# Kernel optimization log

Hardware: AMD Instinct MI355X
Metric: run time of the kernel (lower is better)

Reference implementation:

```python
import jax, jax.numpy as jnp
import numpy as np

N = 100000   # nodes
E = 640000   # edges
D = 128      # feature dim
G = 512      # graphs in the batch


def setup_inputs() -> dict:
    key = jax.random.key(0)
    ks = jax.random.split(key, 6)
    x = jax.random.normal(ks[0], (N, D), dtype=jnp.float32)
    edge_index = jax.random.randint(ks[1], (2, E), 0, N, dtype=jnp.int32)
    batch = jnp.sort(jax.random.randint(ks[2], (N,), 0, G, dtype=jnp.int32))
    scale = 1.0 / np.sqrt(D)
    W0 = jax.random.normal(ks[3], (D, D), dtype=jnp.float32) * scale
    W1 = jax.random.normal(ks[4], (D, D), dtype=jnp.float32) * scale
    W2 = jax.random.normal(ks[5], (D, D), dtype=jnp.float32) * scale
    return {"x": x, "edge_index": edge_index, "batch": batch,
            "W0": W0, "W1": W1, "W2": W2}


def gcn_conv(x, W, row, col, n):
    """GCNConv (bias=False): x' = D^-1/2 (A + I) D^-1/2 (x @ W).
    row/col already include self-loops."""
    xw = x @ W                                              # [N, D]
    deg = jax.ops.segment_sum(jnp.ones_like(col, dtype=x.dtype), col,
                              num_segments=n)               # [N]
    dinv = jnp.where(deg > 0, jax.lax.rsqrt(deg), 0.0)
    norm = dinv[row] * dinv[col]                            # [E+N]
    msgs = norm[:, None] * xw[row]                          # gather + scale
    return jax.ops.segment_sum(msgs, col, num_segments=n)   # scatter-add


def reference(x, edge_index, batch, W0, W1, W2):
    n = x.shape[0]
    loops = jnp.arange(n, dtype=edge_index.dtype)
    row = jnp.concatenate([edge_index[0], loops])
    col = jnp.concatenate([edge_index[1], loops])
    # conv_layers[:-1] (no activation between them in forward)
    x = gcn_conv(x, W0, row, col, n)
    x = gcn_conv(x, W1, row, col, n)
    x = jax.nn.leaky_relu(x, negative_slope=0.01)
    x = gcn_conv(x, W2, row, col, n)
    # global_add_pool over graph ids
    return jax.ops.segment_sum(x, batch, num_segments=G)    # [G, D]
```

## Files before the change

kernel.cpp:

```cpp
#include <hip/hip_runtime.h>
#include <hip/hip_bf16.h>
#include <type_traits>

#define FEAT 128

typedef unsigned int uint32;
typedef unsigned short ushort16;
typedef __attribute__((ext_vector_type(8))) short short8;
typedef __attribute__((ext_vector_type(4))) float v4f;
typedef __attribute__((ext_vector_type(2))) float f32x2;

__device__ __forceinline__ ushort16 f2bf(float f) {
    uint32 u = __float_as_uint(f);
    u += 0x7fffu + ((u >> 16) & 1u);
    return (ushort16)(u >> 16);
}
__device__ __forceinline__ float bflo(uint32 u) { return __uint_as_float(u << 16); }
__device__ __forceinline__ float bfhi(uint32 u) { return __uint_as_float(u & 0xffff0000u); }
__device__ __forceinline__ f32x2 up2(uint32 u) { return (f32x2){bflo(u), bfhi(u)}; }

__global__ __launch_bounds__(256) void hydra_kernel(const int* __restrict__ col,
                                                    int* __restrict__ counts,
                                                    const float* __restrict__ W0,
                                                    const float* __restrict__ W1,
                                                    ushort16* __restrict__ W01t,
                                                    float* __restrict__ Pbuf,
                                                    int histBlocks, int E) {
    int b = blockIdx.x;
    int t = threadIdx.x;
    if (b < histBlocks) {
        int id = b * 256 + t;
        if (id * 4 + 3 < E) {
            int4 c4 = *(const int4*)(col + id * 4);
            atomicAdd(&counts[c4.x], 1);
            atomicAdd(&counts[c4.y], 1);
            atomicAdd(&counts[c4.z], 1);
            atomicAdd(&counts[c4.w], 1);
        } else {
            for (int e = id * 4; e < E; e++) atomicAdd(&counts[col[e]], 1);
        }
    } else if (b < histBlocks + 64) {
        __shared__ float sW0[2][FEAT];
        int wb = b - histBlocks;
        int lk = t >> 7;
        int ncol = t & 127;
        int k = wb * 2 + lk;
        sW0[lk][ncol] = W0[(size_t)k * FEAT + ncol];
        __syncthreads();
        float acc = 0.f;
#pragma unroll 4
        for (int j = 0; j < FEAT; j++)
            acc += sW0[lk][j] * W1[(size_t)j * FEAT + ncol];
        W01t[(size_t)ncol * FEAT + k] = f2bf(acc);
    } else {
        int zb = b - histBlocks - 64;
        float4 z = make_float4(0.f, 0.f, 0.f, 0.f);
        float* p = Pbuf + (size_t)zb * 2048 + t * 8;
        *(float4*)p = z;
        *(float4*)(p + 4) = z;
    }
}

__global__ __launch_bounds__(256) void scan_part(const int* __restrict__ counts,
                                                 int* __restrict__ bsum, int n) {
    __shared__ int s[256];
    int base = blockIdx.x * 1024;
    int t = threadIdx.x;
    int v = 0;
#pragma unroll
    for (int i = 0; i < 4; i++) {
        int idx = base + t * 4 + i;
        if (idx < n) v += counts[idx];
    }
    s[t] = v;
    __syncthreads();
    for (int o = 128; o > 0; o >>= 1) {
        if (t < o) s[t] += s[t + o];
        __syncthreads();
    }
    if (t == 0) bsum[blockIdx.x] = s[0];
}

__global__ __launch_bounds__(256) void scan_final(const int* __restrict__ counts,
                                                  const int* __restrict__ bsum,
                                                  int* __restrict__ off, int* __restrict__ nxt,
                                                  float* __restrict__ dinv, int n, int nb) {
    __shared__ int s[256];
    __shared__ int sb[128];
    int base = blockIdx.x * 1024;
    int t = threadIdx.x;
    if (t < nb) sb[t] = bsum[t];
    int c[4];
    int sum = 0;
#pragma unroll
    for (int i = 0; i < 4; i++) {
        int idx = base + t * 4 + i;
        c[i] = (idx < n) ? counts[idx] : 0;
        sum += c[i];
    }
    int v0 = sum;
    s[t] = sum;
    __syncthreads();
    for (int o = 1; o < 256; o <<= 1) {
        int v = (t >= o) ? s[t - o] : 0;
        __syncthreads();
        s[t] += v;
        __syncthreads();
    }
    int blockBase = 0;
    for (int j = 0; j < blockIdx.x; j++) blockBase += sb[j];
    int excl = s[t] - v0 + blockBase;
#pragma unroll
    for (int i = 0; i < 4; i++) {
        int idx = base + t * 4 + i;
        if (idx < n) {
            off[idx] = excl;
            nxt[idx] = excl;
            dinv[idx] = rsqrtf((float)(c[i] + 1));
        }
        excl += c[i];
    }
    if (blockIdx.x == gridDim.x - 1 && t == 255) off[n] = excl;
}

__global__ void fill_kernel(const int* __restrict__ row, const int* __restrict__ col,
                            int* __restrict__ nxt,
                            int* __restrict__ srcArr, int E) {
    int e = blockIdx.x * 256 + threadIdx.x;
    if (e < E) {
        int c = col[e], r = row[e];
        int p = atomicAdd(&nxt[c], 1);
        __builtin_nontemporal_store(r, &srcArr[p]);
    }
}

template <typename T>
__global__ __launch_bounds__(256) void gemm_mfma(const T* __restrict__ A,
                                                 const ushort16* __restrict__ Wt,
                                                 ushort16* __restrict__ Ch, int n,
                                                 int leaky) {
    const int t = threadIdx.x;
    const int w = t >> 6;
    const int lane = t & 63;
    const int quad = lane >> 4;
    const int l16 = lane & 15;
    const int colBase = (w & 1) * 64;

    short8 wf[4][4];
#pragma unroll
    for (int ct = 0; ct < 4; ct++) {
        const ushort16* wp = Wt + (size_t)(colBase + ct * 16 + l16) * FEAT + quad * 8;
#pragma unroll
        for (int ks = 0; ks < 4; ks++) wf[ct][ks] = *(const short8*)(wp + ks * 32);
    }

    const int nTiles = (n + 15) >> 4;
    const int tStride = gridDim.x * 2;
    int tile = blockIdx.x * 2 + (w >> 1);
    if (tile >= nTiles) return;

    auto loadA = [&](int tl, short8 (&a)[4]) {
        const int row = tl * 16 + l16;
        if (row < n) {
            if constexpr (std::is_same<T, float>::value) {
#pragma unroll
                for (int ks = 0; ks < 4; ks++) {
                    const float* ap = A + (size_t)row * FEAT + quad * 8 + ks * 32;
                    float4 f0 = *(const float4*)ap;
                    float4 f1 = *(const float4*)(ap + 4);
                    short8 v;
                    v[0] = f2bf(f0.x); v[1] = f2bf(f0.y); v[2] = f2bf(f0.z); v[3] = f2bf(f0.w);
                    v[4] = f2bf(f1.x); v[5] = f2bf(f1.y); v[6] = f2bf(f1.z); v[7] = f2bf(f1.w);
                    a[ks] = v;
                }
            } else {
                const ushort16* ap = A + (size_t)row * FEAT + quad * 8;
#pragma unroll
                for (int ks = 0; ks < 4; ks++) a[ks] = *(const short8*)(ap + ks * 32);
            }
        } else {
#pragma unroll
            for (int ks = 0; ks < 4; ks++) a[ks] = (short8)0;
        }
    };

    short8 aCur[4];
    loadA(tile, aCur);

    while (tile < nTiles) {
        const int nextTile = tile + tStride;
        short8 aNxt[4];
        if (nextTile < nTiles) loadA(nextTile, aNxt);

        v4f acc[4];
#pragma unroll
        for (int ct = 0; ct < 4; ct++) acc[ct] = (v4f)0.f;
#pragma unroll
        for (int ct = 0; ct < 4; ct++)
#pragma unroll
            for (int ks = 0; ks < 4; ks++)
                acc[ct] = __builtin_amdgcn_mfma_f32_16x16x32_bf16(wf[ct][ks], aCur[ks], acc[ct], 0, 0, 0);

        const int row = tile * 16 + l16;
        if (row < n) {
#pragma unroll
            for (int ct = 0; ct < 4; ct++) {
                float p0 = acc[ct][0], p1 = acc[ct][1], p2 = acc[ct][2], p3 = acc[ct][3];
                if (leaky) {
                    p0 = (p0 >= 0.f) ? p0 : 0.01f * p0;
                    p1 = (p1 >= 0.f) ? p1 : 0.01f * p1;
                    p2 = (p2 >= 0.f) ? p2 : 0.01f * p2;
                    p3 = (p3 >= 0.f) ? p3 : 0.01f * p3;
                }
                uint2 o;
                o.x = (uint32)f2bf(p0) | ((uint32)f2bf(p1) << 16);
                o.y = (uint32)f2bf(p2) | ((uint32)f2bf(p3) << 16);
                *(uint2*)(Ch + (size_t)row * FEAT + colBase + ct * 16 + quad * 4) = o;
            }
        }

        tile = nextTile;
#pragma unroll
        for (int ks = 0; ks < 4; ks++) aCur[ks] = aNxt[ks];
    }
}

__global__ __launch_bounds__(256) void gather_kernel(const int* __restrict__ off,
                                                     const int* __restrict__ srcArr,
                                                     const float* __restrict__ dinv,
                                                     const ushort16* __restrict__ XWh,
                                                     ushort16* __restrict__ Hh, int n,
                                                     int leaky) {
    int node = blockIdx.x * 4 + (threadIdx.x >> 6);
    if (node >= n) return;
    int lane = threadIdx.x & 63;
    int grp = lane >> 4;
    int l16 = lane & 15;
    float dc = dinv[node];
    const uint4* table = (const uint4*)XWh;

    f32x2 acc[4];
    if (grp == 0) {
        uint4 v = table[(size_t)node * 16 + l16];
        f32x2 w0 = (f32x2){dc * dc, dc * dc};
        acc[0] = w0 * up2(v.x);
        acc[1] = w0 * up2(v.y);
        acc[2] = w0 * up2(v.z);
        acc[3] = w0 * up2(v.w);
    } else {
#pragma unroll
        for (int j = 0; j < 4; j++) acc[j] = (f32x2){0.f, 0.f};
    }

    int s = off[node], e = off[node + 1];
    int i = s + grp;
    for (; i + 4 < e; i += 8) {
        int r0 = srcArr[i];
        int r1 = srcArr[i + 4];
        uint4 u0 = table[(size_t)r0 * 16 + l16];
        uint4 u1 = table[(size_t)r1 * 16 + l16];
        float f0 = dc * dinv[r0];
        float f1 = dc * dinv[r1];
        f32x2 n0 = (f32x2){f0, f0};
        f32x2 n1 = (f32x2){f1, f1};
        acc[0] += n0 * up2(u0.x);
        acc[1] += n0 * up2(u0.y);
        acc[2] += n0 * up2(u0.z);
        acc[3] += n0 * up2(u0.w);
        acc[0] += n1 * up2(u1.x);
        acc[1] += n1 * up2(u1.y);
        acc[2] += n1 * up2(u1.z);
        acc[3] += n1 * up2(u1.w);
    }
    if (i < e) {
        int r0 = srcArr[i];
        uint4 u0 = table[(size_t)r0 * 16 + l16];
        float f0 = dc * dinv[r0];
        f32x2 n0 = (f32x2){f0, f0};
        acc[0] += n0 * up2(u0.x);
        acc[1] += n0 * up2(u0.y);
        acc[2] += n0 * up2(u0.z);
        acc[3] += n0 * up2(u0.w);
    }

    float b[8] = {acc[0].x, acc[0].y, acc[1].x, acc[1].y,
                  acc[2].x, acc[2].y, acc[3].x, acc[3].y};
#pragma unroll
    for (int j = 0; j < 8; j++) {
        b[j] += __shfl_xor(b[j], 16);
        b[j] += __shfl_xor(b[j], 32);
    }

    if (grp == 0) {
        if (leaky) {
#pragma unroll
            for (int j = 0; j < 8; j++) b[j] = (b[j] >= 0.f) ? b[j] : 0.01f * b[j];
        }
        uint4 o;
        o.x = (uint32)f2bf(b[0]) | ((uint32)f2bf(b[1]) << 16);
        o.y = (uint32)f2bf(b[2]) | ((uint32)f2bf(b[3]) << 16);
        o.z = (uint32)f2bf(b[4]) | ((uint32)f2bf(b[5]) << 16);
        o.w = (uint32)f2bf(b[6]) | ((uint32)f2bf(b[7]) << 16);
        *(uint4*)(Hh + (size_t)node * FEAT + l16 * 8) = o;
    }
}

__global__ __launch_bounds__(128) void pool_kernel(const ushort16* __restrict__ H,
                                                   const int* __restrict__ batch,
                                                   float* __restrict__ P, int n) {
    int t = threadIdx.x;
    int i0 = blockIdx.x * 64;
    if (i0 >= n) return;
    int i1 = min(i0 + 64, n);
    float acc = 0.f;
    int g = batch[i0];
    for (int i = i0; i < i1; i++) {
        int b = batch[i];
        if (b != g) {
            atomicAdd(&P[(size_t)g * FEAT + t], acc);
            acc = 0.f;
            g = b;
        }
        uint32 u = (uint32)(unsigned short)H[(size_t)i * FEAT + t];
        acc += __uint_as_float(u << 16);
    }
    atomicAdd(&P[(size_t)g * FEAT + t], acc);
}

__global__ __launch_bounds__(128) void pgemm_kernel(const float* __restrict__ P,
                                                    const float* __restrict__ W2,
                                                    float* __restrict__ out) {
    __shared__ float sP[FEAT];
    const int g = blockIdx.x;
    const int t = threadIdx.x;
    sP[t] = P[(size_t)g * FEAT + t];
    __syncthreads();
    float o = 0.f;
#pragma unroll 4
    for (int k = 0; k < FEAT; k++) o += sP[k] * W2[(size_t)k * FEAT + t];
    out[(size_t)g * FEAT + t] = o;
}

extern "C" void kernel_launch(void* const* d_in, const int* in_sizes, int n_in,
                              void* d_out, int out_size, void* d_ws, size_t ws_size,
                              hipStream_t stream) {
    const float* x = (const float*)d_in[0];
    const int* ei = (const int*)d_in[1];
    const int* batch = (const int*)d_in[2];
    const float* W0 = (const float*)d_in[3];
    const float* W1 = (const float*)d_in[4];
    const float* W2 = (const float*)d_in[5];
    float* out = (float*)d_out;

    const int N = in_sizes[0] / FEAT;
    const int E = in_sizes[1] / 2;
    const int G = out_size / FEAT;

    const int* rowI = ei;
    const int* colI = ei + E;

    char* ws = (char*)d_ws;
    auto take = [&](size_t bytes) {
        char* p = ws;
        ws += (bytes + 15) & ~(size_t)15;
        return p;
    };
    int* counts    = (int*)take((size_t)N * 4);
    int* off       = (int*)take((size_t)(N + 1) * 4);
    int* nxt       = (int*)take((size_t)N * 4);
    float* dinv    = (float*)take((size_t)N * 4);
    int* bsum      = (int*)take(128 * 4);
    int* srcArr    = (int*)take((size_t)E * 4);
    ushort16* W01t = (ushort16*)take((size_t)16384 * 2);
    float* Pbuf    = (float*)take((size_t)G * FEAT * 4);
    ushort16* bufA = (ushort16*)take((size_t)N * FEAT * 2);
    ushort16* bufB = (ushort16*)take((size_t)N * FEAT * 2);

    const int nb = (N + 1023) / 1024;
    const int eb = (E + 255) / 256;

    hipMemsetAsync(counts, 0, (size_t)N * 4, stream);
    const int histBlocks = (E + 1023) / 1024;
    hydra_kernel<<<histBlocks + 64 + 32, 256, 0, stream>>>(
        colI, counts, W0, W1, W01t, Pbuf, histBlocks, E);

    scan_part<<<nb, 256, 0, stream>>>(counts, bsum, N);
    scan_final<<<nb, 256, 0, stream>>>(counts, bsum, off, nxt, dinv, N, nb);
    fill_kernel<<<eb, 256, 0, stream>>>(rowI, colI, nxt, srcArr, E);

    const int gatBlocks = (N + 3) / 4;

    gemm_mfma<float><<<1024, 256, 0, stream>>>(x, W01t, bufA, N, 0);
    gather_kernel<<<gatBlocks, 256, 0, stream>>>(off, srcArr, dinv, bufA, bufB, N, 0);
    gather_kernel<<<gatBlocks, 256, 0, stream>>>(off, srcArr, dinv, bufB, bufA, N, 1);
    gather_kernel<<<gatBlocks, 256, 0, stream>>>(off, srcArr, dinv, bufA, bufB, N, 0);
    pool_kernel<<<(N + 63) / 64, 128, 0, stream>>>(bufB, batch, Pbuf, N);
    pgemm_kernel<<<G, 128, 0, stream>>>(Pbuf, W2, out);
}
```

Baseline: 365.2 us.

## Split feature table into two column halves to shrink gather working set

Stores the GEMM output and each propagation buffer as two separate N×64 column halves instead of one N×128 array. Each gather pass now runs twice, once per half, using 8 lanes per row and 8 edge groups per wave. The aim is a smaller random-access working set per pass (about 12.8 MB instead of 25.6 MB of bf16), so more of it stays cache-resident. The cost is twice as many gather launches, with the CSR indices and dinv read twice. The pool kernel is adapted to the split layout.

```diff
diff --git a/kernel.cpp b/kernel.cpp
--- a/kernel.cpp
+++ b/kernel.cpp
@@ -1,6 +1,5 @@
 #include <hip/hip_runtime.h>
 #include <hip/hip_bf16.h>
-#include <type_traits>
 
 #define FEAT 128
 
@@ -134,17 +133,17 @@
     }
 }
 
-template <typename T>
-__global__ __launch_bounds__(256) void gemm_mfma(const T* __restrict__ A,
+__global__ __launch_bounds__(256) void gemm_mfma(const float* __restrict__ A,
                                                  const ushort16* __restrict__ Wt,
-                                                 ushort16* __restrict__ Ch, int n,
-                                                 int leaky) {
+                                                 ushort16* __restrict__ Ch, int n) {
     const int t = threadIdx.x;
     const int w = t >> 6;
     const int lane = t & 63;
     const int quad = lane >> 4;
     const int l16 = lane & 15;
-    const int colBase = (w & 1) * 64;
+    const int h = w & 1;
+    const int colBase = h * 64;
+    ushort16* halfC = Ch + (size_t)h * n * 64;
 
     short8 wf[4][4];
 #pragma unroll
@@ -162,21 +161,15 @@
     auto loadA = [&](int tl, short8 (&a)[4]) {
         const int row = tl * 16 + l16;
         if (row < n) {
-            if constexpr (std::is_same<T, float>::value) {
-#pragma unroll
-                for (int ks = 0; ks < 4; ks++) {
-                    const float* ap = A + (size_t)row * FEAT + quad * 8 + ks * 32;
-                    float4 f0 = *(const float4*)ap;
-                    float4 f1 = *(const float4*)(ap + 4);
-                    short8 v;
-                    v[0] = f2bf(f0.x); v[1] = f2bf(f0.y); v[2] = f2bf(f0.z); v[3] = f2bf(f0.w);
-                    v[4] = f2bf(f1.x); v[5] = f2bf(f1.y); v[6] = f2bf(f1.z); v[7] = f2bf(f1.w);
-                    a[ks] = v;
-                }
-            } else {
-                const ushort16* ap = A + (size_t)row * FEAT + quad * 8;
-#pragma unroll
-                for (int ks = 0; ks < 4; ks++) a[ks] = *(const short8*)(ap + ks * 32);
+#pragma unroll
+            for (int ks = 0; ks < 4; ks++) {
+                const float* ap = A + (size_t)row * FEAT + quad * 8 + ks * 32;
+                float4 f0 = *(const float4*)ap;
+                float4 f1 = *(const float4*)(ap + 4);
+                short8 v;
+                v[0] = f2bf(f0.x); v[1] = f2bf(f0.y); v[2] = f2bf(f0.z); v[3] = f2bf(f0.w);
+                v[4] = f2bf(f1.x); v[5] = f2bf(f1.y); v[6] = f2bf(f1.z); v[7] = f2bf(f1.w);
+                a[ks] = v;
             }
         } else {
 #pragma unroll
@@ -205,17 +198,10 @@
         if (row < n) {
 #pragma unroll
             for (int ct = 0; ct < 4; ct++) {
-                float p0 = acc[ct][0], p1 = acc[ct][1], p2 = acc[ct][2], p3 = acc[ct][3];
-                if (leaky) {
-                    p0 = (p0 >= 0.f) ? p0 : 0.01f * p0;
-                    p1 = (p1 >= 0.f) ? p1 : 0.01f * p1;
-                    p2 = (p2 >= 0.f) ? p2 : 0.01f * p2;
-                    p3 = (p3 >= 0.f) ? p3 : 0.01f * p3;
-                }
                 uint2 o;
-                o.x = (uint32)f2bf(p0) | ((uint32)f2bf(p1) << 16);
-                o.y = (uint32)f2bf(p2) | ((uint32)f2bf(p3) << 16);
-                *(uint2*)(Ch + (size_t)row * FEAT + colBase + ct * 16 + quad * 4) = o;
+                o.x = (uint32)f2bf(acc[ct][0]) | ((uint32)f2bf(acc[ct][1]) << 16);
+                o.y = (uint32)f2bf(acc[ct][2]) | ((uint32)f2bf(acc[ct][3]) << 16);
+                *(uint2*)(halfC + (size_t)row * 64 + ct * 16 + quad * 4) = o;
             }
         }
 
@@ -228,20 +214,19 @@
 __global__ __launch_bounds__(256) void gather_kernel(const int* __restrict__ off,
                                                      const int* __restrict__ srcArr,
                                                      const float* __restrict__ dinv,
-                                                     const ushort16* __restrict__ XWh,
-                                                     ushort16* __restrict__ Hh, int n,
+                                                     const uint4* __restrict__ T,
+                                                     uint4* __restrict__ O, int n,
                                                      int leaky) {
     int node = blockIdx.x * 4 + (threadIdx.x >> 6);
     if (node >= n) return;
     int lane = threadIdx.x & 63;
-    int grp = lane >> 4;
-    int l16 = lane & 15;
+    int grp = lane >> 3;
+    int l8 = lane & 7;
     float dc = dinv[node];
-    const uint4* table = (const uint4*)XWh;
 
     f32x2 acc[4];
     if (grp == 0) {
-        uint4 v = table[(size_t)node * 16 + l16];
+        uint4 v = T[(size_t)node * 8 + l8];
         f32x2 w0 = (f32x2){dc * dc, dc * dc};
         acc[0] = w0 * up2(v.x);
         acc[1] = w0 * up2(v.y);
@@ -254,11 +239,11 @@
 
     int s = off[node], e = off[node + 1];
     int i = s + grp;
-    for (; i + 4 < e; i += 8) {
+    for (; i + 8 < e; i += 16) {
         int r0 = srcArr[i];
-        int r1 = srcArr[i + 4];
-        uint4 u0 = table[(size_t)r0 * 16 + l16];
-        uint4 u1 = table[(size_t)r1 * 16 + l16];
+        int r1 = srcArr[i + 8];
+        uint4 u0 = T[(size_t)r0 * 8 + l8];
+        uint4 u1 = T[(size_t)r1 * 8 + l8];
         float f0 = dc * dinv[r0];
         float f1 = dc * dinv[r1];
         f32x2 n0 = (f32x2){f0, f0};
@@ -274,7 +259,7 @@
     }
     if (i < e) {
         int r0 = srcArr[i];
-        uint4 u0 = table[(size_t)r0 * 16 + l16];
+        uint4 u0 = T[(size_t)r0 * 8 + l8];
         float f0 = dc * dinv[r0];
         f32x2 n0 = (f32x2){f0, f0};
         acc[0] += n0 * up2(u0.x);
@@ -287,6 +272,7 @@
                   acc[2].x, acc[2].y, acc[3].x, acc[3].y};
 #pragma unroll
     for (int j = 0; j < 8; j++) {
+        b[j] += __shfl_xor(b[j], 8);
         b[j] += __shfl_xor(b[j], 16);
         b[j] += __shfl_xor(b[j], 32);
     }
@@ -301,7 +287,7 @@
         o.y = (uint32)f2bf(b[2]) | ((uint32)f2bf(b[3]) << 16);
         o.z = (uint32)f2bf(b[4]) | ((uint32)f2bf(b[5]) << 16);
         o.w = (uint32)f2bf(b[6]) | ((uint32)f2bf(b[7]) << 16);
-        *(uint4*)(Hh + (size_t)node * FEAT + l16 * 8) = o;
+        O[(size_t)node * 8 + l8] = o;
     }
 }
 
@@ -309,6 +295,8 @@
                                                    const int* __restrict__ batch,
                                                    float* __restrict__ P, int n) {
     int t = threadIdx.x;
+    const ushort16* Hh = H + (size_t)(t >> 6) * n * 64;
+    int f = t & 63;
     int i0 = blockIdx.x * 64;
     if (i0 >= n) return;
     int i1 = min(i0 + 64, n);
@@ -321,7 +309,7 @@
             acc = 0.f;
             g = b;
         }
-        uint32 u = (uint32)(unsigned short)H[(size_t)i * FEAT + t];
+        uint32 u = (uint32)(unsigned short)Hh[(size_t)i * 64 + f];
         acc += __uint_as_float(u << 16);
     }
     atomicAdd(&P[(size_t)g * FEAT + t], acc);
@@ -389,11 +377,18 @@
     fill_kernel<<<eb, 256, 0, stream>>>(rowI, colI, nxt, srcArr, E);
 
     const int gatBlocks = (N + 3) / 4;
-
-    gemm_mfma<float><<<1024, 256, 0, stream>>>(x, W01t, bufA, N, 0);
-    gather_kernel<<<gatBlocks, 256, 0, stream>>>(off, srcArr, dinv, bufA, bufB, N, 0);
-    gather_kernel<<<gatBlocks, 256, 0, stream>>>(off, srcArr, dinv, bufB, bufA, N, 1);
-    gather_kernel<<<gatBlocks, 256, 0, stream>>>(off, srcArr, dinv, bufA, bufB, N, 0);
+    uint4* A0 = (uint4*)bufA;
+    uint4* A1 = (uint4*)(bufA + (size_t)N * 64);
+    uint4* B0 = (uint4*)bufB;
+    uint4* B1 = (uint4*)(bufB + (size_t)N * 64);
+
+    gemm_mfma<<<1024, 256, 0, stream>>>(x, W01t, bufA, N);
+    gather_kernel<<<gatBlocks, 256, 0, stream>>>(off, srcArr, dinv, A0, B0, N, 0);
+    gather_kernel<<<gatBlocks, 256, 0, stream>>>(off, srcArr, dinv, A1, B1, N, 0);
+    gather_kernel<<<gatBlocks, 256, 0, stream>>>(off, srcArr, dinv, B0, A0, N, 1);
+    gather_kernel<<<gatBlocks, 256, 0, stream>>>(off, srcArr, dinv, B1, A1, N, 1);
+    gather_kernel<<<gatBlocks, 256, 0, stream>>>(off, srcArr, dinv, A0, B0, N, 0);
+    gather_kernel<<<gatBlocks, 256, 0, stream>>>(off, srcArr, dinv, A1, B1, N, 0);
     pool_kernel<<<(N + 63) / 64, 128, 0, stream>>>(bufB, batch, Pbuf, N);
     pgemm_kernel<<<G, 128, 0, stream>>>(Pbuf, W2, out);
 }
```

Measured after the change: 454.6 us. +24.5%, slower.

## Fuse CSR fill and first GEMM into one interleaved horizontal kernel

Applied to the files above, without the earlier changes.

Merges the edge fill (atomic bucket placement) and the fp32→bf16 MFMA GEMM into a single launch, with blocks interleaved 2 GEMM : 5 fill per group of 7. The two kernels are independent, so running them together lets the latency-bound atomic scatter overlap with the compute/bandwidth-bound GEMM and saves one launch. The cost is a more complex block mapping and a larger grid (3584 blocks) with a hardcoded GEMM block count. The unused leaky path and template are removed.

```diff
diff --git a/kernel.cpp b/kernel.cpp
--- a/kernel.cpp
+++ b/kernel.cpp
@@ -1,6 +1,5 @@
 #include <hip/hip_runtime.h>
 #include <hip/hip_bf16.h>
-#include <type_traits>
 
 #define FEAT 128
 
@@ -123,23 +122,31 @@
     if (blockIdx.x == gridDim.x - 1 && t == 255) off[n] = excl;
 }
 
-__global__ void fill_kernel(const int* __restrict__ row, const int* __restrict__ col,
-                            int* __restrict__ nxt,
-                            int* __restrict__ srcArr, int E) {
-    int e = blockIdx.x * 256 + threadIdx.x;
-    if (e < E) {
-        int c = col[e], r = row[e];
-        int p = atomicAdd(&nxt[c], 1);
-        __builtin_nontemporal_store(r, &srcArr[p]);
-    }
-}
-
-template <typename T>
-__global__ __launch_bounds__(256) void gemm_mfma(const T* __restrict__ A,
-                                                 const ushort16* __restrict__ Wt,
-                                                 ushort16* __restrict__ Ch, int n,
-                                                 int leaky) {
+__global__ __launch_bounds__(256) void gemmfill_kernel(const float* __restrict__ A,
+                                                       const ushort16* __restrict__ Wt,
+                                                       ushort16* __restrict__ Ch, int n,
+                                                       const int* __restrict__ row,
+                                                       const int* __restrict__ col,
+                                                       int* __restrict__ nxt,
+                                                       int* __restrict__ srcArr, int E) {
+    const int b = blockIdx.x;
+    const int r7 = b % 7;
+    const int g7 = b / 7;
     const int t = threadIdx.x;
+
+    if (r7 >= 2) {
+        int fb = g7 * 5 + (r7 - 2);
+        int e = fb * 256 + t;
+        if (e < E) {
+            int c = col[e], r = row[e];
+            int p = atomicAdd(&nxt[c], 1);
+            __builtin_nontemporal_store(r, &srcArr[p]);
+        }
+        return;
+    }
+
+    const int gb = g7 * 2 + r7;
+    const int GEMM_BLOCKS = 1024;
     const int w = t >> 6;
     const int lane = t & 63;
     const int quad = lane >> 4;
@@ -155,28 +162,22 @@
     }
 
     const int nTiles = (n + 15) >> 4;
-    const int tStride = gridDim.x * 2;
-    int tile = blockIdx.x * 2 + (w >> 1);
+    const int tStride = GEMM_BLOCKS * 2;
+    int tile = gb * 2 + (w >> 1);
     if (tile >= nTiles) return;
 
     auto loadA = [&](int tl, short8 (&a)[4]) {
-        const int row = tl * 16 + l16;
-        if (row < n) {
-            if constexpr (std::is_same<T, float>::value) {
-#pragma unroll
-                for (int ks = 0; ks < 4; ks++) {
-                    const float* ap = A + (size_t)row * FEAT + quad * 8 + ks * 32;
-                    float4 f0 = *(const float4*)ap;
-                    float4 f1 = *(const float4*)(ap + 4);
-                    short8 v;
-                    v[0] = f2bf(f0.x); v[1] = f2bf(f0.y); v[2] = f2bf(f0.z); v[3] = f2bf(f0.w);
-                    v[4] = f2bf(f1.x); v[5] = f2bf(f1.y); v[6] = f2bf(f1.z); v[7] = f2bf(f1.w);
-                    a[ks] = v;
-                }
-            } else {
-                const ushort16* ap = A + (size_t)row * FEAT + quad * 8;
-#pragma unroll
-                for (int ks = 0; ks < 4; ks++) a[ks] = *(const short8*)(ap + ks * 32);
+        const int rowi = tl * 16 + l16;
+        if (rowi < n) {
+#pragma unroll
+            for (int ks = 0; ks < 4; ks++) {
+                const float* ap = A + (size_t)rowi * FEAT + quad * 8 + ks * 32;
+                float4 f0 = *(const float4*)ap;
+                float4 f1 = *(const float4*)(ap + 4);
+                short8 v;
+                v[0] = f2bf(f0.x); v[1] = f2bf(f0.y); v[2] = f2bf(f0.z); v[3] = f2bf(f0.w);
+                v[4] = f2bf(f1.x); v[5] = f2bf(f1.y); v[6] = f2bf(f1.z); v[7] = f2bf(f1.w);
+                a[ks] = v;
             }
         } else {
 #pragma unroll
@@ -201,21 +202,14 @@
             for (int ks = 0; ks < 4; ks++)
                 acc[ct] = __builtin_amdgcn_mfma_f32_16x16x32_bf16(wf[ct][ks], aCur[ks], acc[ct], 0, 0, 0);
 
-        const int row = tile * 16 + l16;
-        if (row < n) {
+        const int rowi = tile * 16 + l16;
+        if (rowi < n) {
 #pragma unroll
             for (int ct = 0; ct < 4; ct++) {
-                float p0 = acc[ct][0], p1 = acc[ct][1], p2 = acc[ct][2], p3 = acc[ct][3];
-                if (leaky) {
-                    p0 = (p0 >= 0.f) ? p0 : 0.01f * p0;
-                    p1 = (p1 >= 0.f) ? p1 : 0.01f * p1;
-                    p2 = (p2 >= 0.f) ? p2 : 0.01f * p2;
-                    p3 = (p3 >= 0.f) ? p3 : 0.01f * p3;
-                }
                 uint2 o;
-                o.x = (uint32)f2bf(p0) | ((uint32)f2bf(p1) << 16);
-                o.y = (uint32)f2bf(p2) | ((uint32)f2bf(p3) << 16);
-                *(uint2*)(Ch + (size_t)row * FEAT + colBase + ct * 16 + quad * 4) = o;
+                o.x = (uint32)f2bf(acc[ct][0]) | ((uint32)f2bf(acc[ct][1]) << 16);
+                o.y = (uint32)f2bf(acc[ct][2]) | ((uint32)f2bf(acc[ct][3]) << 16);
+                *(uint2*)(Ch + (size_t)rowi * FEAT + colBase + ct * 16 + quad * 4) = o;
             }
         }
 
@@ -377,7 +371,6 @@
     ushort16* bufB = (ushort16*)take((size_t)N * FEAT * 2);
 
     const int nb = (N + 1023) / 1024;
-    const int eb = (E + 255) / 256;
 
     hipMemsetAsync(counts, 0, (size_t)N * 4, stream);
     const int histBlocks = (E + 1023) / 1024;
@@ -386,11 +379,11 @@
 
     scan_part<<<nb, 256, 0, stream>>>(counts, bsum, N);
     scan_final<<<nb, 256, 0, stream>>>(counts, bsum, off, nxt, dinv, N, nb);
-    fill_kernel<<<eb, 256, 0, stream>>>(rowI, colI, nxt, srcArr, E);
+
+    gemmfill_kernel<<<512 * 7, 256, 0, stream>>>(x, W01t, bufA, N,
+                                                 rowI, colI, nxt, srcArr, E);
 
     const int gatBlocks = (N + 3) / 4;
-
-    gemm_mfma<float><<<1024, 256, 0, stream>>>(x, W01t, bufA, N, 0);
     gather_kernel<<<gatBlocks, 256, 0, stream>>>(off, srcArr, dinv, bufA, bufB, N, 0);
     gather_kernel<<<gatBlocks, 256, 0, stream>>>(off, srcArr, dinv, bufB, bufA, N, 1);
     gather_kernel<<<gatBlocks, 256, 0, stream>>>(off, srcArr, dinv, bufA, bufB, N, 0);
```

New measurement: 340.5 us. 1.07x faster.
